# Kernel optimization log

Hardware: AMD Instinct MI355X
Metric: run time of the kernel (lower is better)

## Reference

```python
import math
import jax, jax.numpy as jnp
import numpy as np

N_KINDS = 8
D_MODEL = 256
B_FEAT = 24  # Fourier bands; MLP input dim is 2*B_FEAT
SIGMA = 8.0


def setup_inputs() -> dict:
    key = jax.random.key(0)
    ks = jax.random.split(key, 8)
    N, S = 32, 2048
    values = jax.random.normal(ks[0], (N, S, 1), dtype=jnp.float32)
    kinds = jax.random.randint(ks[1], (N, S), 0, N_KINDS, dtype=jnp.int32)
    # Frozen Fourier projection matrix (torch: randn(in_dim, B) * sigma, requires_grad=False)
    Bmat = jax.random.normal(ks[2], (1, B_FEAT), dtype=jnp.float32) * SIGMA
    # Kind embedding table
    kind_emb = jax.random.normal(ks[3], (N_KINDS, D_MODEL), dtype=jnp.float32) * 0.02
    # Per-kind two-layer MLP params
    W1 = jax.random.normal(ks[4], (N_KINDS, 2 * B_FEAT, D_MODEL), dtype=jnp.float32) / math.sqrt(2 * B_FEAT)
    b1 = jnp.zeros((N_KINDS, D_MODEL), dtype=jnp.float32)
    W2 = jax.random.normal(ks[5], (N_KINDS, D_MODEL, D_MODEL), dtype=jnp.float32) / math.sqrt(D_MODEL)
    b2 = jnp.zeros((N_KINDS, D_MODEL), dtype=jnp.float32)
    return {"values": values, "kinds": kinds, "Bmat": Bmat,
            "kind_emb": kind_emb, "W1": W1, "b1": b1, "W2": W2, "b2": b2}


def reference(values, kinds, Bmat, kind_emb, W1, b1, W2, b2):
    N, S, _ = values.shape
    T = N * S
    d = kind_emb.shape[-1]
    # Fourier features: [T, 2B]
    y = (2.0 * math.pi) * values.reshape(T, 1) @ Bmat  # [T, B]
    ff = jnp.concatenate([jnp.sin(y), jnp.cos(y)], axis=-1)  # [T, 2B]
    kinds_flat = kinds.reshape(T)
    out = jnp.zeros((T, d), dtype=values.dtype)
    # kinds partition the tokens, so masked combine == the torch scatter-assign
    for k in range(kind_emb.shape[0]):
        h = jax.nn.gelu(ff @ W1[k] + b1[k], approximate=False)  # torch GELU is exact erf
        o = h @ W2[k] + b2[k]  # [T, d]
        out = jnp.where((kinds_flat == k)[:, None], o, out)
    return out.reshape(N, S, d) + kind_emb[kinds]
```

## Files before the change

### kernel.cpp

```cpp
#include <hip/hip_runtime.h>
#include <hip/hip_bf16.h>
#include <math.h>


#define NK 8
#define DM 256
#define TMAX 65536
#define NBLK 256
#define W1PK 16384
#define W2PK 65536
#define LDSTRIDE 262

typedef __attribute__((ext_vector_type(8))) short   s16x8;
typedef __attribute__((ext_vector_type(8))) __bf16  bf16x8;
typedef __attribute__((ext_vector_type(4))) float   f32x4;
typedef __attribute__((ext_vector_type(2))) float   f32x2;

__device__ __align__(16) int g_counts[NK * 32];
__device__ int   g_bucket[(size_t)NK * TMAX];
__device__ __align__(16) short g_W1p[(size_t)NK * W1PK];
__device__ __align__(16) short g_W2p[(size_t)NK * W2PK];

static __device__ __forceinline__ short f2bf(float f) {
    __hip_bfloat16 h = __float2bfloat16(f);
    return __builtin_bit_cast(short, h);
}

static __device__ __forceinline__ short pkbf(float f) {
    unsigned u = __builtin_bit_cast(unsigned, f);
    return (short)((u + 0x8000u) >> 16);
}

static __device__ __forceinline__ f32x4 mfma16(s16x8 a, s16x8 b, f32x4 c) {
    return __builtin_amdgcn_mfma_f32_16x16x32_bf16(
        __builtin_bit_cast(bf16x8, a), __builtin_bit_cast(bf16x8, b), c, 0, 0, 0);
}

static __device__ __forceinline__ float gelu_fast(float x) {
    float t1 = x * x;
    float m  = fmaf(0.0713548162726f, t1, 1.59576912161f);
    float z  = m * x;
    float e  = __expf(-z);
    return x * __frcp_rn(1.0f + e);
}

__global__ __launch_bounds__(256) void prep_kernel(const float* __restrict__ W1,
                                                   const float* __restrict__ W2,
                                                   const int* __restrict__ kinds, int T) {
    const int tid = threadIdx.x;
    const int bid = blockIdx.x;
    if (bid < 80) {
        __shared__ float ld[32 * LDSTRIDE];
        const int isW1 = (bid >= 64);
        int kind, kt;
        if (isW1) { kind = (bid - 64) >> 1; kt = (bid - 64) & 1; }
        else      { kind = bid >> 3;        kt = bid & 7; }
        #pragma unroll
        for (int i = 0; i < 8; ++i) {
            int f = tid + i * 256;
            int row = f >> 6, col = (f & 63) * 4;
            int kk = kt * 32 + row;
            f32x4 v = (f32x4){0.f, 0.f, 0.f, 0.f};
            if (isW1) {
                if (kk < 48) v = *(const f32x4*)(W1 + ((size_t)kind * 48 + kk) * DM + col);
            } else {
                v = *(const f32x4*)(W2 + ((size_t)kind * DM + kk) * DM + col);
            }
            float* dst = &ld[row * LDSTRIDE + col];
            *(f32x2*)dst       = (f32x2){v[0], v[1]};
            *(f32x2*)(dst + 2) = (f32x2){v[2], v[3]};
        }
        __syncthreads();
        short* outp = isW1 ? (g_W1p + (size_t)kind * W1PK) : (g_W2p + (size_t)kind * W2PK);
        #pragma unroll
        for (int i = 0; i < 4; ++i) {
            int g = tid + i * 256;
            int ntile = g >> 6, l = g & 63;
            int kk0 = (l >> 4) * 8, n = ntile * 16 + (l & 15);
            s16x8 v;
            #pragma unroll
            for (int j = 0; j < 8; ++j) v[j] = f2bf(ld[(kk0 + j) * LDSTRIDE + n]);
            *(s16x8*)(outp + ((size_t)(kt * 16 + ntile) * 64 + l) * 8) = v;
        }
    } else {
        __shared__ int wcnt[4][NK];
        __shared__ int base_s[NK];
        const int b = bid - 80;
        const int wave = tid >> 6, lane = tid & 63;
        int t = b * 256 + tid;
        int k = (t < T) ? kinds[t] : -1;
        int rank = 0;
        #pragma unroll
        for (int kk = 0; kk < NK; ++kk) {
            unsigned long long m = __ballot(k == kk);
            if (lane == 0) wcnt[wave][kk] = __popcll(m);
            if (k == kk) rank = __popcll(m & ((1ull << lane) - 1ull));
        }
        __syncthreads();
        if (tid < NK) {
            int ws = 0;
            #pragma unroll
            for (int w = 0; w < 4; ++w) { int c = wcnt[w][tid]; wcnt[w][tid] = ws; ws += c; }
            base_s[tid] = atomicAdd(&g_counts[tid * 32], ws);
        }
        __syncthreads();
        if (k >= 0)
            g_bucket[(size_t)k * T + base_s[k] + wcnt[wave][k] + rank] = t;
    }
}

__global__ __launch_bounds__(512, 4) void fproj_gemm(
    const float* __restrict__ values, const float* __restrict__ Bmat,
    const float* __restrict__ kind_emb, const float* __restrict__ b1,
    const float* __restrict__ b2, float* __restrict__ out, int T)
{
    int cnts[NK];
    #pragma unroll
    for (int i = 0; i < NK; ++i) cnts[i] = g_counts[i * 32];
    const int bid = blockIdx.x;
    const int tid = threadIdx.x;
    int k = -1, m0 = 0, cum = 0, cnt = 0;
    #pragma unroll
    for (int kk = 0; kk < NK; ++kk) {
        int tk = (cnts[kk] + 63) >> 6;
        if (k < 0 && bid < cum + tk) { k = kk; m0 = (bid - cum) * 64; cnt = cnts[kk]; }
        cum += tk;
    }
    if (k < 0) return;
    const int valid = min(64, cnt - m0);
    const int* buck = g_bucket + (size_t)k * T + m0;

    __shared__ short Hpack[16384];

    const int wv   = tid >> 6;
    const int lane = tid & 63;
    const int quad = lane >> 4;
    const int cl   = lane & 15;

    const s16x8* B1p = (const s16x8*)(g_W1p + (size_t)k * W1PK);
    s16x8 bfp[2][2];
    #pragma unroll
    for (int kt = 0; kt < 2; ++kt)
        #pragma unroll
        for (int nt = 0; nt < 2; ++nt) bfp[kt][nt] = B1p[(kt * 16 + wv * 2 + nt) * 64 + lane];
    float bias1[2], addc[2];
    #pragma unroll
    for (int nt = 0; nt < 2; ++nt) {
        int c = wv * 32 + nt * 16 + cl;
        bias1[nt] = b1[k * DM + c];
        addc[nt]  = b2[k * DM + c] + kind_emb[k * DM + c];
    }

    float vm[4];
    #pragma unroll
    for (int mt = 0; mt < 4; ++mt) {
        int row = mt * 16 + cl;
        vm[mt] = (row < valid) ? values[buck[row]] : 0.0f;
    }
    float bb0[8], bb1[8];
    const float add0 = (quad == 3) ? 0.25f : 0.0f;
    #pragma unroll
    for (int j = 0; j < 8; ++j) {
        int b0 = (quad == 3) ? j : quad * 8 + j;
        bb0[j] = Bmat[b0];
        int b1i = min(8 * (quad + 1) + j, 23);
        bb1[j] = Bmat[b1i];
    }
    s16x8 a0[4], a1[4];
    #pragma unroll
    for (int mt = 0; mt < 4; ++mt) {
        float v = vm[mt];
        #pragma unroll
        for (int j = 0; j < 8; ++j) {
            float r0 = __builtin_amdgcn_fractf(fmaf(v, bb0[j], add0));
            a0[mt][j] = pkbf(__builtin_amdgcn_sinf(r0));
            float r1 = __builtin_amdgcn_fractf(fmaf(v, bb1[j], 0.25f));
            float c1 = __builtin_amdgcn_sinf(r1);
            a1[mt][j] = pkbf((quad < 2) ? c1 : 0.0f);
        }
    }

    f32x4 acc[4][2];
    #pragma unroll
    for (int mt = 0; mt < 4; ++mt)
        #pragma unroll
        for (int nt = 0; nt < 2; ++nt) acc[mt][nt] = (f32x4){0.f, 0.f, 0.f, 0.f};
    #pragma unroll
    for (int kt = 0; kt < 2; ++kt) {
        #pragma unroll
        for (int mt = 0; mt < 4; ++mt) {
            s16x8 a = kt ? a1[mt] : a0[mt];
            #pragma unroll
            for (int nt = 0; nt < 2; ++nt) acc[mt][nt] = mfma16(a, bfp[kt][nt], acc[mt][nt]);
        }
    }

    const s16x8* B2p = (const s16x8*)(g_W2p + (size_t)k * W2PK);
    s16x8 bf2[2];
    #pragma unroll
    for (int nt = 0; nt < 2; ++nt) bf2[nt] = B2p[(wv * 2 + nt) * 64 + lane];

    #pragma unroll
    for (int nt = 0; nt < 2; ++nt) {
        int c = wv * 32 + nt * 16 + cl;
        int kt2 = c >> 5, q2 = (c >> 3) & 3, j2 = c & 7;
        #pragma unroll
        for (int mt = 0; mt < 4; ++mt) {
            short* hp = Hpack + (kt2 * 4 + mt) * 512 + q2 * 128 + j2;
            #pragma unroll
            for (int r = 0; r < 4; ++r) {
                int m = quad * 4 + r;
                float h = gelu_fast(acc[mt][nt][r] + bias1[nt]);
                hp[m * 8] = pkbf(h);
            }
        }
    }
    __syncthreads();

    f32x4 acc2[4][2];
    #pragma unroll
    for (int mt = 0; mt < 4; ++mt)
        #pragma unroll
        for (int nt = 0; nt < 2; ++nt) acc2[mt][nt] = (f32x4){0.f, 0.f, 0.f, 0.f};
    const s16x8* Hp  = (const s16x8*)Hpack;
    #pragma unroll
    for (int kt = 0; kt < 8; ++kt) {
        s16x8 bfn[2];
        if (kt < 7) {
            #pragma unroll
            for (int nt = 0; nt < 2; ++nt)
                bfn[nt] = B2p[((kt + 1) * 16 + wv * 2 + nt) * 64 + lane];
        }
        s16x8 am[4];
        #pragma unroll
        for (int mt = 0; mt < 4; ++mt) am[mt] = Hp[(kt * 4 + mt) * 64 + lane];
        #pragma unroll
        for (int mt = 0; mt < 4; ++mt)
            #pragma unroll
            for (int nt = 0; nt < 2; ++nt) acc2[mt][nt] = mfma16(am[mt], bf2[nt], acc2[mt][nt]);
        #pragma unroll
        for (int nt = 0; nt < 2; ++nt) bf2[nt] = bfn[nt];
    }

    #pragma unroll
    for (int mt = 0; mt < 4; ++mt)
        #pragma unroll
        for (int r = 0; r < 4; ++r) {
            int row = mt * 16 + quad * 4 + r;
            if (row < valid) {
                size_t ro = (size_t)buck[row] * DM;
                #pragma unroll
                for (int nt = 0; nt < 2; ++nt) {
                    int c = wv * 32 + nt * 16 + cl;
                    __builtin_nontemporal_store(acc2[mt][nt][r] + addc[nt], out + ro + c);
                }
            }
        }
}

extern "C" void kernel_launch(void* const* d_in, const int* in_sizes, int n_in,
                              void* d_out, int out_size, void* d_ws, size_t ws_size,
                              hipStream_t stream) {
    const float* values   = (const float*)d_in[0];
    const int*   kinds    = (const int*)  d_in[1];
    const float* Bmat     = (const float*)d_in[2];
    const float* kind_emb = (const float*)d_in[3];
    const float* W1       = (const float*)d_in[4];
    const float* b1       = (const float*)d_in[5];
    const float* W2       = (const float*)d_in[6];
    const float* b2       = (const float*)d_in[7];
    float* out = (float*)d_out;
    const int T = in_sizes[0];

    static void* cnt_addr = nullptr;
    if (!cnt_addr) (void)hipGetSymbolAddress(&cnt_addr, HIP_SYMBOL(g_counts));
    hipMemsetAsync(cnt_addr, 0, sizeof(int) * NK * 32, stream);

    prep_kernel<<<dim3(80 + NBLK), dim3(256), 0, stream>>>(W1, W2, kinds, T);
    fproj_gemm<<<dim3(T / 64 + NK), dim3(512), 0, stream>>>(values, Bmat, kind_emb,
                                                            b1, b2, out, T);
}
```

Measured before the change: 121.1 us.

## Preload all W2 fragments before GELU and interleave GEMM2 with stores per row tile

Loads every W2 B-fragment for the wave (8 k-steps by 2 n-tiles) into registers before the GELU/LDS-pack phase, so the global loads overlap the GELU work and the barrier. It also reorders GEMM2 so each 16-row tile is accumulated over all k and stored at once, which lets output stores overlap later MFMAs and shrinks the accumulator footprint. The cost is more VGPRs held for the B fragments (16 x 8 shorts), which may lower occupancy.

Measured after the change: 123.2 us. No clear change (+1.8%).

```diff
diff --git a/kernel.cpp b/kernel.cpp
--- a/kernel.cpp
+++ b/kernel.cpp
@@ -196,9 +196,12 @@
     }
 
     const s16x8* B2p = (const s16x8*)(g_W2p + (size_t)k * W2PK);
-    s16x8 bf2[2];
-    #pragma unroll
-    for (int nt = 0; nt < 2; ++nt) bf2[nt] = B2p[(wv * 2 + nt) * 64 + lane];
+    s16x8 bf2[8][2];
+    #pragma unroll
+    for (int kt = 0; kt < 8; ++kt)
+        #pragma unroll
+        for (int nt = 0; nt < 2; ++nt)
+            bf2[kt][nt] = B2p[(kt * 16 + wv * 2 + nt) * 64 + lane];
 
     #pragma unroll
     for (int nt = 0; nt < 2; ++nt) {
@@ -217,33 +220,18 @@
     }
     __syncthreads();
 
-    f32x4 acc2[4][2];
-    #pragma unroll
-    for (int mt = 0; mt < 4; ++mt)
-        #pragma unroll
-        for (int nt = 0; nt < 2; ++nt) acc2[mt][nt] = (f32x4){0.f, 0.f, 0.f, 0.f};
-    const s16x8* Hp  = (const s16x8*)Hpack;
-    #pragma unroll
-    for (int kt = 0; kt < 8; ++kt) {
-        s16x8 bfn[2];
-        if (kt < 7) {
-            #pragma unroll
-            for (int nt = 0; nt < 2; ++nt)
-                bfn[nt] = B2p[((kt + 1) * 16 + wv * 2 + nt) * 64 + lane];
-        }
-        s16x8 am[4];
-        #pragma unroll
-        for (int mt = 0; mt < 4; ++mt) am[mt] = Hp[(kt * 4 + mt) * 64 + lane];
-        #pragma unroll
-        for (int mt = 0; mt < 4; ++mt)
-            #pragma unroll
-            for (int nt = 0; nt < 2; ++nt) acc2[mt][nt] = mfma16(am[mt], bf2[nt], acc2[mt][nt]);
-        #pragma unroll
-        for (int nt = 0; nt < 2; ++nt) bf2[nt] = bfn[nt];
-    }
-
-    #pragma unroll
-    for (int mt = 0; mt < 4; ++mt)
+    const s16x8* Hp = (const s16x8*)Hpack;
+    #pragma unroll
+    for (int mt = 0; mt < 4; ++mt) {
+        f32x4 a2[2];
+        a2[0] = (f32x4){0.f, 0.f, 0.f, 0.f};
+        a2[1] = (f32x4){0.f, 0.f, 0.f, 0.f};
+        #pragma unroll
+        for (int kt = 0; kt < 8; ++kt) {
+            s16x8 am = Hp[(kt * 4 + mt) * 64 + lane];
+            a2[0] = mfma16(am, bf2[kt][0], a2[0]);
+            a2[1] = mfma16(am, bf2[kt][1], a2[1]);
+        }
         #pragma unroll
         for (int r = 0; r < 4; ++r) {
             int row = mt * 16 + quad * 4 + r;
@@ -252,10 +240,11 @@
                 #pragma unroll
                 for (int nt = 0; nt < 2; ++nt) {
                     int c = wv * 32 + nt * 16 + cl;
-                    __builtin_nontemporal_store(acc2[mt][nt][r] + addc[nt], out + ro + c);
+                    __builtin_nontemporal_store(a2[nt][r] + addc[nt], out + ro + c);
                 }
             }
         }
+    }
 }
 
 extern "C" void kernel_launch(void* const* d_in, const int* in_sizes, int n_in,
```
